# Kernel tuning notes

Measured on AMD Instinct MI355X. Metric: run time of the kernel, lower is better.

The kernel has to match this reference:

```python
import jax, jax.numpy as jnp
import numpy as np

N, D = 512, 256          # n candidates, span_emb_size
R = 4                    # num relation types / etypes
FF = 512                 # mention_linker_ffnn_size, depth 1
L = 2                    # ieg_bignn_hidden_layers
DH = D // 2              # GraphConvolution output size


def setup_inputs() -> dict:
    key = jax.random.key(0)
    ks = jax.random.split(key, 12)
    s = lambda fan_in: 1.0 / np.sqrt(fan_in)
    return {
        "candidate_embs": jax.random.normal(ks[0], (N, D), jnp.float32),
        # relation scorer FFNN: 3D -> FF -> R
        "W_sc0": jax.random.normal(ks[1], (3 * D, FF), jnp.float32) * s(3 * D),
        "b_sc0": jnp.zeros((FF,), jnp.float32),
        "W_sc1": jax.random.normal(ks[2], (FF, R), jnp.float32) * s(FF),
        "b_sc1": jnp.zeros((R,), jnp.float32),
        # BiGCN: per-layer, per-relation fw/bw GraphConvolution D -> D//2
        "W_fw": jax.random.normal(ks[3], (L, R, D, DH), jnp.float32) * s(D),
        "b_fw": jnp.zeros((L, R, DH), jnp.float32),
        "W_bw": jax.random.normal(ks[4], (L, R, D, DH), jnp.float32) * s(D),
        "b_bw": jnp.zeros((L, R, DH), jnp.float32),
        # per-layer linear1: D -> D
        "W_lin": jax.random.normal(ks[5], (L, D, D), jnp.float32) * s(D),
        "b_lin": jnp.zeros((L, D), jnp.float32),
    }


def reference(candidate_embs, W_sc0, b_sc0, W_sc1, b_sc1,
              W_fw, b_fw, W_bw, b_bw, W_lin, b_lin):
    n, d = candidate_embs.shape
    # --- get_pair_embs: [n, n, 3d] = cat(src, target, src*target) ---
    src = jnp.broadcast_to(candidate_embs[None, :, :], (n, n, d))   # row i varies j
    tgt = jnp.broadcast_to(candidate_embs[:, None, :], (n, n, d))
    pair = jnp.concatenate([src, tgt, src * tgt], axis=-1)          # [n, n, 3d]
    # --- relation scorer FFNN (ReLU hidden, dropout=0 at inference) ---
    h = jax.nn.relu(jnp.einsum('ijk,kf->ijf', pair, W_sc0) + b_sc0)
    scores = jnp.einsum('ijf,fr->ijr', h, W_sc1) + b_sc1            # [n, n, R]
    probs = jax.nn.softmax(scores, axis=-1)
    # --- adjs_from_preds: detach, zero diagonal; bw = fw^T ---
    probs = jax.lax.stop_gradient(probs)
    A = jnp.moveaxis(probs, -1, 0)                                   # [R, n, n]
    eye = jnp.eye(n, dtype=bool)
    A = jnp.where(eye[None, :, :], 0.0, A)
    AT = jnp.swapaxes(A, 1, 2)
    # --- BiGCN: L layers of multi-relation bi-directional GCN ---
    x = candidate_embs
    for l in range(L):
        sup_fw = jnp.einsum('nd,rde->rne', x, W_fw[l])               # [R, n, DH]
        sup_bw = jnp.einsum('nd,rde->rne', x, W_bw[l])
        fw = jnp.einsum('rij,rje->rie', A, sup_fw) + b_fw[l][:, None, :]
        bw = jnp.einsum('rij,rje->rie', AT, sup_bw) + b_bw[l][:, None, :]
        outs = jnp.concatenate([bw, fw], axis=-1)                    # [R, n, D]
        x = jax.nn.relu(outs.sum(axis=0)) @ W_lin[l] + b_lin[l] + x  # residual
    return x
```

## Files before the change

kernel.cpp:

```cpp
#include <hip/hip_runtime.h>
#include <hip/hip_bf16.h>

using f32x4  = __attribute__((ext_vector_type(4))) float;
using bf16x8 = __attribute__((ext_vector_type(8))) short;

__device__ __forceinline__ unsigned short f2bf(float f) {
    union { __hip_bfloat16 h; unsigned short u; } cv;
    cv.h = __float2bfloat16(f);
    return cv.u;
}
__device__ __forceinline__ unsigned int pack2bf(float lo, float hi) {
    float2 t; t.x = lo; t.y = hi;
    union { __hip_bfloat162 h; unsigned int u; } cv;
    cv.h = __float22bfloat162_rn(t);
    return cv.u;
}
__device__ __forceinline__ float bf2f(unsigned short u) {
    return __uint_as_float((unsigned)u << 16);
}
__device__ __forceinline__ void ld_lds16(const unsigned short* g, unsigned short* l) {
    __builtin_amdgcn_global_load_lds(
        (const __attribute__((address_space(1))) unsigned int*)g,
        (__attribute__((address_space(3))) unsigned int*)l, 16, 0, 0);
}

__global__ __launch_bounds__(512) void prep_kernel(
        const float* __restrict__ E, const float* __restrict__ Wsc0, const float* __restrict__ Wsc1,
        const float* __restrict__ Wfw, const float* __restrict__ bfw,
        const float* __restrict__ Wbw, const float* __restrict__ bbw,
        const float* __restrict__ Wlin,
        unsigned short* __restrict__ E16, unsigned short* __restrict__ W0p,
        unsigned short* __restrict__ WabP,
        unsigned short* __restrict__ WcatT, unsigned short* __restrict__ WlinT,
        float* __restrict__ bsumS, unsigned short* __restrict__ W1p) {
    const int NE = 131072, NW0 = 131072, NWAB = 262144, NCAT = 524288, NLIN = 131072, NW1P = 8192;
    const int total = NE + NW0 + NWAB + NCAT + NLIN + NW1P + 512;
    for (int idx = blockIdx.x * 512 + threadIdx.x; idx < total; idx += 512 * 512) {
        int t = idx;
        if (t < NE) { E16[t] = f2bf(E[t]); continue; }
        t -= NE;
        if (t < NW0) {
            int k = t >> 9, f = t & 511;
            int w = f >> 6, nb = (f >> 4) & 3, l15 = f & 15;
            int kk = k >> 5, l4 = (k >> 3) & 3, e = k & 7;
            W0p[((((w * 4 + nb) * 8 + kk) * 64) + l4 * 16 + l15) * 8 + e] = f2bf(Wsc0[(512 + k) * 512 + f]);
            continue;
        }
        t -= NW0;
        if (t < NWAB) {
            int r = t >> 9, col = t & 511;
            int k = r & 255;
            int fcol = (r < 256) ? col : (512 + col);
            int wf = fcol >> 6, nb = (fcol >> 4) & 3, l15 = fcol & 15;
            int kk = k >> 5, l4 = (k >> 3) & 3, e = k & 7;
            WabP[((((wf * 4 + nb) * 8 + kk) * 64) + l4 * 16 + l15) * 8 + e] = f2bf(Wsc0[r * 512 + col]);
            continue;
        }
        t -= NWAB;
        if (t < NCAT) {
            int e = t & 127, k = (t >> 7) & 255, r = (t >> 15) & 3, d = (t >> 17) & 1, l = t >> 18;
            const float* src = (d == 0) ? Wfw : Wbw;
            float v = src[((l * 4 + r) * 256 + k) * 128 + e];
            WcatT[(l * 1024 + d * 512 + r * 128 + e) * 256 + k] = f2bf(v);
            continue;
        }
        t -= NCAT;
        if (t < NLIN) {
            int d = t & 255, f = (t >> 8) & 255, l = t >> 16;
            WlinT[(l * 256 + d) * 256 + f] = f2bf(Wlin[(l * 256 + f) * 256 + d]);
            continue;
        }
        t -= NLIN;
        if (t < NW1P) {
            int e = t & 7, lane = (t >> 3) & 63, kap = t >> 9;
            int fp = kap * 32 + (lane >> 4) * 8 + e;
            int w = fp >> 6, q = (fp >> 2) & 15, nb = fp & 3;
            int f = w * 64 + nb * 16 + q;
            int r = lane & 15;
            W1p[t] = (r < 4) ? f2bf(Wsc1[f * 4 + r]) : (unsigned short)0;
            continue;
        }
        t -= NW1P;
        {
            int f = t & 255, l = t >> 8;
            float s = 0.f;
            if (f < 128) { for (int r = 0; r < 4; ++r) s += bbw[(l * 4 + r) * 128 + f]; }
            else         { for (int r = 0; r < 4; ++r) s += bfw[(l * 4 + r) * 128 + (f - 128)]; }
            bsumS[l * 256 + f] = s;
        }
    }
}

__global__ __launch_bounds__(512) void uv_kernel(const unsigned short* __restrict__ E16,
                                                 const unsigned short* __restrict__ WabP,
                                                 const float* __restrict__ bsc0,
                                                 unsigned short* __restrict__ Upk,
                                                 float* __restrict__ V) {
    __shared__ unsigned short sE[32 * 256];
    const int jt = blockIdx.x;
    const int tid = threadIdx.x, lane = tid & 63, w = tid >> 6;
    const int l15 = lane & 15, l4 = lane >> 4;
#pragma unroll
    for (int it = 0; it < 2; ++it) {
        int u = it * 512 + tid;
        int row = u >> 5, slot = u & 31;
        uint4 v = *(const uint4*)(E16 + (jt * 32 + row) * 256 + slot * 8);
        *(uint4*)((char*)sE + row * 512 + ((slot * 16) ^ ((row & 7) << 4))) = v;
    }
    __syncthreads();
    const bf16x8* Wab8 = (const bf16x8*)WabP;
    f32x4 acc[2][8];
#pragma unroll
    for (int a_ = 0; a_ < 2; ++a_)
#pragma unroll
        for (int b_ = 0; b_ < 8; ++b_) acc[a_][b_] = (f32x4){0.f, 0.f, 0.f, 0.f};
#pragma unroll
    for (int kk = 0; kk < 8; ++kk) {
        bf16x8 af[2];
#pragma unroll
        for (int mbl = 0; mbl < 2; ++mbl) {
            int row = mbl * 16 + l15;
            af[mbl] = *(const bf16x8*)((char*)sE + row * 512 + ((kk * 64 + l4 * 16) ^ ((row & 7) << 4)));
        }
#pragma unroll
        for (int nb = 0; nb < 8; ++nb) {
            int wf = 2 * w + (nb >> 2);
            bf16x8 bfr = Wab8[((wf * 4 + (nb & 3)) * 8 + kk) * 64 + lane];
#pragma unroll
            for (int mbl = 0; mbl < 2; ++mbl)
                acc[mbl][nb] = __builtin_amdgcn_mfma_f32_16x16x32_bf16(af[mbl], bfr, acc[mbl][nb], 0, 0, 0);
        }
    }
#pragma unroll
    for (int mbl = 0; mbl < 2; ++mbl) {
        int j_base = jt * 32 + mbl * 16 + l4 * 4;
#pragma unroll
        for (int nb8 = 0; nb8 < 8; ++nb8) {
            int f_g = (2 * w + (nb8 >> 2)) * 64 + (nb8 & 3) * 16 + l15;
            if (f_g < 512) {
                float b0f = bsc0[f_g];
                ushort4 o;
                o.x = f2bf(acc[mbl][nb8][0] + b0f);
                o.y = f2bf(acc[mbl][nb8][1] + b0f);
                o.z = f2bf(acc[mbl][nb8][2] + b0f);
                o.w = f2bf(acc[mbl][nb8][3] + b0f);
                int jtp = j_base >> 6, mbp = (j_base >> 4) & 3;
                int wp = f_g >> 6, nbp = (f_g >> 4) & 3;
                int lanep = l4 * 16 + l15;
                *(ushort4*)(Upk + ((((jtp * 8 + wp) * 4 + mbp) * 2 + (nbp >> 1)) * 64 + lanep) * 8 + (nbp & 1) * 4) = o;
            } else {
                int fv = f_g - 512;
#pragma unroll
                for (int reg = 0; reg < 4; ++reg)
                    V[(j_base + reg) * 512 + fv] = acc[mbl][nb8][reg];
            }
        }
    }
}

__global__ __launch_bounds__(512, 2) void pair_kernel(
    const unsigned short* __restrict__ E16, const unsigned short* __restrict__ W0p,
    const unsigned short* __restrict__ Upk, const float* __restrict__ V,
    const unsigned short* __restrict__ W1p, const float* __restrict__ b1,
    unsigned short* __restrict__ A16) {

    __shared__ unsigned short bufL[2 * 64 * 256];
    __shared__ unsigned short Bbuf[2][8][4][512];
    __shared__ float vrow[2][512];
    __shared__ float scoresL[2][256];

    const int i0 = blockIdx.x * 2, i1 = i0 + 1;
    const int jt = blockIdx.y;
    const int j0 = jt * 64;
    const int tid = threadIdx.x;
    const int lane = tid & 63;
    const int w = tid >> 6;
    const int l15 = lane & 15, l4 = lane >> 4;

    uint4 uq[4][2];
#pragma unroll
    for (int mb = 0; mb < 4; ++mb)
#pragma unroll
        for (int nbh = 0; nbh < 2; ++nbh)
            uq[mb][nbh] = *(const uint4*)(Upk + ((((jt * 8 + w) * 4 + mb) * 2 + nbh) * 64 + lane) * 8);
    vrow[0][tid] = V[i0 * 512 + tid];
    vrow[1][tid] = V[i1 * 512 + tid];
    if (tid < 256) { scoresL[0][tid] = b1[tid & 3]; scoresL[1][tid] = b1[tid & 3]; }

    {
        int m = tid >> 3;
        int s = tid & 7;
        const bf16x8* ejp  = (const bf16x8*)(E16 + (j0 + m) * 256 + s * 8);
        const bf16x8* ei0p = (const bf16x8*)(E16 + i0 * 256 + s * 8);
        const bf16x8* ei1p = (const bf16x8*)(E16 + i1 * 256 + s * 8);
        char* base = (char*)bufL;
#pragma unroll
        for (int c = 0; c < 4; ++c) {
            bf16x8 ej = ejp[c * 8], e0 = ei0p[c * 8], e1 = ei1p[c * 8];
            uint4 v0, v1;
            unsigned* p0 = (unsigned*)&v0;
            unsigned* p1 = (unsigned*)&v1;
#pragma unroll
            for (int e2 = 0; e2 < 4; ++e2) {
                float jl = bf2f((unsigned short)ej[e2 * 2]), jh = bf2f((unsigned short)ej[e2 * 2 + 1]);
                p0[e2] = pack2bf(jl * bf2f((unsigned short)e0[e2 * 2]), jh * bf2f((unsigned short)e0[e2 * 2 + 1]));
                p1[e2] = pack2bf(jl * bf2f((unsigned short)e1[e2 * 2]), jh * bf2f((unsigned short)e1[e2 * 2 + 1]));
            }
            int off = m * 512 + ((s * 16 + c * 128) ^ ((m & 7) << 4));
            *(uint4*)(base + off) = v0;
            *(uint4*)(base + 32768 + off) = v1;
        }
    }

    f32x4 acc0[4][4], acc1[4][4];
#pragma unroll
    for (int mb = 0; mb < 4; ++mb)
#pragma unroll
        for (int nbh = 0; nbh < 2; ++nbh) {
            const unsigned short* us = (const unsigned short*)&uq[mb][nbh];
#pragma unroll
            for (int h = 0; h < 2; ++h) {
                int nb = nbh * 2 + h;
                float v0f = vrow[0][w * 64 + nb * 16 + l15];
                float v1f = vrow[1][w * 64 + nb * 16 + l15];
#pragma unroll
                for (int reg = 0; reg < 4; ++reg) {
                    float uu = bf2f(us[h * 4 + reg]);
                    acc0[mb][nb][reg] = uu + v0f;
                    acc1[mb][nb][reg] = uu + v1f;
                }
            }
        }
    __syncthreads();

#pragma unroll
    for (int nb = 0; nb < 4; ++nb)
        ld_lds16(W0p + ((((w * 4 + nb) * 8 + 0) * 64) + lane) * 8, &Bbuf[0][w][nb][0]);
#pragma unroll
    for (int nb = 0; nb < 4; ++nb)
        ld_lds16(W0p + ((((w * 4 + nb) * 8 + 1) * 64) + lane) * 8, &Bbuf[1][w][nb][0]);

    const char* pbase = (const char*)bufL;
#define PKK(KK, WSTR)                                                                                  \
    {                                                                                                  \
        asm volatile("s_waitcnt " WSTR ::: "memory");                                                  \
        bf16x8 bfr[4];                                                                                 \
        {                                                                                              \
            const char* bsrc = (const char*)(&Bbuf[(KK) & 1][w][0][0]);                                \
            _Pragma("unroll") for (int nb = 0; nb < 4; ++nb)                                           \
                bfr[nb] = *(const bf16x8*)(bsrc + nb * 1024 + lane * 16);                              \
        }                                                                                              \
        bf16x8 afr[4];                                                                                 \
        _Pragma("unroll") for (int mb = 0; mb < 4; ++mb) {                                             \
            int row = mb * 16 + l15;                                                                   \
            afr[mb] = *(const bf16x8*)(pbase + row * 512 + (((KK) * 64 + l4 * 16) ^ ((row & 7) << 4)));\
        }                                                                                              \
        asm volatile("s_waitcnt lgkmcnt(0)" ::: "memory");                                             \
        __builtin_amdgcn_sched_barrier(0);                                                             \
        if ((KK) < 6) {                                                                                \
            _Pragma("unroll") for (int nb = 0; nb < 4; ++nb)                                           \
                ld_lds16(W0p + ((((w * 4 + nb) * 8 + (KK) + 2) * 64) + lane) * 8,                      \
                         &Bbuf[(KK) & 1][w][nb][0]);                                                   \
        }                                                                                              \
        _Pragma("unroll") for (int mb = 0; mb < 4; ++mb)                                               \
            _Pragma("unroll") for (int nb = 0; nb < 4; ++nb)                                           \
                acc0[mb][nb] = __builtin_amdgcn_mfma_f32_16x16x32_bf16(afr[mb], bfr[nb],               \
                                                                       acc0[mb][nb], 0, 0, 0);        \
        _Pragma("unroll") for (int mb = 0; mb < 4; ++mb) {                                             \
            int row = mb * 16 + l15;                                                                   \
            afr[mb] = *(const bf16x8*)(pbase + 32768 + row * 512 +                                     \
                                       (((KK) * 64 + l4 * 16) ^ ((row & 7) << 4)));                    \
        }                                                                                              \
        _Pragma("unroll") for (int mb = 0; mb < 4; ++mb)                                               \
            _Pragma("unroll") for (int nb = 0; nb < 4; ++nb)                                           \
                acc1[mb][nb] = __builtin_amdgcn_mfma_f32_16x16x32_bf16(afr[mb], bfr[nb],               \
                                                                       acc1[mb][nb], 0, 0, 0);        \
    }
    PKK(0, "vmcnt(4)")
    PKK(1, "vmcnt(4)")
    PKK(2, "vmcnt(4)")
    PKK(3, "vmcnt(4)")
    PKK(4, "vmcnt(4)")
    PKK(5, "vmcnt(4)")
    PKK(6, "vmcnt(4)")
    PKK(7, "vmcnt(0)")
#undef PKK
    __syncthreads();

    char* hb = (char*)bufL;
    const bf16x8* W1p8 = (const bf16x8*)W1p;
    bf16x8 w1f[2];
#pragma unroll
    for (int kl = 0; kl < 2; ++kl) w1f[kl] = W1p8[(w * 2 + kl) * 64 + lane];

#pragma unroll
    for (int ii = 0; ii < 2; ++ii) {
#pragma unroll
        for (int mb = 0; mb < 4; ++mb)
#pragma unroll
            for (int reg = 0; reg < 4; ++reg) {
                int rl = mb * 16 + l4 * 4 + reg;
                f32x4* A = (ii == 0) ? &acc0[mb][0] : &acc1[mb][0];
                float h0 = fmaxf(A[0][reg], 0.f);
                float h1 = fmaxf(A[1][reg], 0.f);
                float h2 = fmaxf(A[2][reg], 0.f);
                float h3 = fmaxf(A[3][reg], 0.f);
                uint2 val;
                val.x = pack2bf(h0, h1);
                val.y = pack2bf(h2, h3);
                *(uint2*)(hb + rl * 1024 + ((w * 128 + l15 * 8) ^ ((rl & 7) << 4))) = val;
            }
        __syncthreads();
        f32x4 accS[4];
#pragma unroll
        for (int mb = 0; mb < 4; ++mb) {
            accS[mb] = (f32x4){0.f, 0.f, 0.f, 0.f};
            int rl = mb * 16 + l15;
#pragma unroll
            for (int kl = 0; kl < 2; ++kl) {
                bf16x8 ha = *(const bf16x8*)(hb + rl * 1024 + (((w * 2 + kl) * 64 + l4 * 16) ^ ((rl & 7) << 4)));
                accS[mb] = __builtin_amdgcn_mfma_f32_16x16x32_bf16(ha, w1f[kl], accS[mb], 0, 0, 0);
            }
        }
        if (l15 < 4) {
#pragma unroll
            for (int mb = 0; mb < 4; ++mb)
#pragma unroll
                for (int reg = 0; reg < 4; ++reg)
                    atomicAdd(&scoresL[ii][(mb * 16 + l4 * 4 + reg) * 4 + l15], accS[mb][reg]);
        }
        __syncthreads();
    }

    if (tid < 128) {
        int ii = tid >> 6, m = tid & 63;
        int j = j0 + m, ic = i0 + ii;
        float s0 = scoresL[ii][m * 4 + 0], s1 = scoresL[ii][m * 4 + 1];
        float sA = scoresL[ii][m * 4 + 2], sB = scoresL[ii][m * 4 + 3];
        float mx = fmaxf(fmaxf(s0, s1), fmaxf(sA, sB));
        float e0 = __expf(s0 - mx), e1 = __expf(s1 - mx), e2 = __expf(sA - mx), e3 = __expf(sB - mx);
        float inv = 1.f / (e0 + e1 + e2 + e3);
        float p_[4] = {e0 * inv, e1 * inv, e2 * inv, e3 * inv};
        if (j == ic) { p_[0] = p_[1] = p_[2] = p_[3] = 0.f; }
#pragma unroll
        for (int r = 0; r < 4; ++r)
            A16[(r * 512 + ic) * 512 + j] = f2bf(p_[r]);
    }
}

template<int K>
__device__ __forceinline__ void stageP(unsigned short* lds, const unsigned short* g, int ldg, int tid) {
    constexpr int SLOTS = K / 8;
#pragma unroll
    for (int it = 0; it < (32 * SLOTS) / 256; ++it) {
        int u = it * 256 + tid;
        int row = u / SLOTS, slot = u % SLOTS;
        uint4 v = *(const uint4*)(g + row * ldg + slot * 8);
        *(uint4*)((char*)lds + row * (K * 2) + ((slot * 16) ^ ((row & 7) << 4))) = v;
    }
}
__device__ __forceinline__ void stage64(unsigned short* lds, const unsigned short* g, int ldg, int tid) {
#pragma unroll
    for (int it = 0; it < 8; ++it) {
        int u = it * 256 + tid;
        int row = u >> 5, slot = u & 31;
        uint4 v = *(const uint4*)(g + row * ldg + slot * 8);
        *(uint4*)((char*)lds + row * 512 + ((slot * 16) ^ ((row & 7) << 4))) = v;
    }
}
template<int K>
__device__ __forceinline__ bf16x8 fragP(const unsigned short* lds, int row, int kc, int l4) {
    return *(const bf16x8*)((const char*)lds + row * (K * 2) + ((((kc * 4 + l4) * 16) ^ ((row & 7) << 4))));
}

__global__ __launch_bounds__(256) void c1_kernel(const unsigned short* __restrict__ WcatT,
                                                 const unsigned short* __restrict__ x16,
                                                 unsigned short* __restrict__ supT,
                                                 const unsigned short* __restrict__ A16,
                                                 unsigned short* __restrict__ AT16, int l) {
    __shared__ unsigned short lA[32 * 256], lB[32 * 256];
    int tid = threadIdx.x;
    if (blockIdx.y >= 16) {
        auto t = (unsigned short(*)[65])lA;
        int job = (blockIdx.y - 16) * 32 + blockIdx.x;
        int r = job >> 6, ty = (job >> 3) & 7, tx = job & 7;
        const unsigned short* src = A16 + (r * 512 + ty * 64) * 512 + tx * 64;
        unsigned short* dst = AT16 + (r * 512 + tx * 64) * 512 + ty * 64;
#pragma unroll
        for (int it = 0; it < 2; ++it) {
            int u = it * 256 + tid, row = u >> 3, c8 = (u & 7) * 8;
            uint4 v = *(const uint4*)(src + row * 512 + c8);
            const unsigned short* p = (const unsigned short*)&v;
#pragma unroll
            for (int e = 0; e < 8; ++e) t[c8 + e][row] = p[e];
        }
        __syncthreads();
#pragma unroll
        for (int it = 0; it < 2; ++it) {
            int u = it * 256 + tid, row = u >> 3, c8 = (u & 7) * 8;
            uint4 v; unsigned short* p = (unsigned short*)&v;
#pragma unroll
            for (int e = 0; e < 8; ++e) p[e] = t[row][c8 + e];
            *(uint4*)(dst + row * 512 + c8) = v;
        }
        return;
    }
    int c0 = blockIdx.x * 32, jt0 = blockIdx.y * 32;
    int lane = tid & 63, w = tid >> 6;
    int wr = (w >> 1) * 16, wc = (w & 1) * 16;
    int l15 = lane & 15, l4 = lane >> 4;
    stageP<256>(lA, WcatT + l * 262144 + c0 * 256, 256, tid);
    stageP<256>(lB, x16 + jt0 * 256, 256, tid);
    __syncthreads();
    f32x4 a0 = {0.f,0.f,0.f,0.f}, a1 = {0.f,0.f,0.f,0.f};
#pragma unroll
    for (int kc = 0; kc < 8; kc += 2) {
        a0 = __builtin_amdgcn_mfma_f32_16x16x32_bf16(fragP<256>(lA, wr + l15, kc, l4),
                                                     fragP<256>(lB, wc + l15, kc, l4), a0, 0, 0, 0);
        a1 = __builtin_amdgcn_mfma_f32_16x16x32_bf16(fragP<256>(lA, wr + l15, kc + 1, l4),
                                                     fragP<256>(lB, wc + l15, kc + 1, l4), a1, 0, 0, 0);
    }
    f32x4 acc = a0 + a1;
#pragma unroll
    for (int reg = 0; reg < 4; ++reg) {
        int c = c0 + wr + l4 * 4 + reg;
        int j = jt0 + wc + l15;
        supT[c * 512 + j] = f2bf(acc[reg]);
    }
}

__global__ __launch_bounds__(256) void c2_kernel(const unsigned short* __restrict__ A16,
                                                 const unsigned short* __restrict__ AT16,
                                                 const unsigned short* __restrict__ supT,
                                                 float* __restrict__ Pc2) {
    __shared__ unsigned short lA[64 * 256], lB[64 * 256];
    int i0 = blockIdx.x * 64, f0 = blockIdx.y * 64;
    int s = blockIdx.z, r = s >> 1, kh = s & 1;
    bool bw = (f0 < 128);
    int e0 = bw ? f0 : (f0 - 128);
    const unsigned short* Am = bw ? AT16 : A16;
    int tid = threadIdx.x, lane = tid & 63, w = tid >> 6;
    int wr = (w >> 1) * 32, wc = (w & 1) * 32;
    int l15 = lane & 15, l4 = lane >> 4;
    stage64(lA, Am + (r * 512 + i0) * 512 + kh * 256, 512, tid);
    stage64(lB, supT + ((bw ? 512 : 0) + r * 128 + e0) * 512 + kh * 256, 512, tid);
    __syncthreads();
    f32x4 acc[2][2];
#pragma unroll
    for (int a_ = 0; a_ < 2; ++a_)
#pragma unroll
        for (int b_ = 0; b_ < 2; ++b_) acc[a_][b_] = (f32x4){0.f, 0.f, 0.f, 0.f};
#pragma unroll
    for (int kc = 0; kc < 8; ++kc) {
        bf16x8 af[2], bf_[2];
#pragma unroll
        for (int mb = 0; mb < 2; ++mb) af[mb] = fragP<256>(lA, wr + mb * 16 + l15, kc, l4);
#pragma unroll
        for (int nb = 0; nb < 2; ++nb) bf_[nb] = fragP<256>(lB, wc + nb * 16 + l15, kc, l4);
#pragma unroll
        for (int mb = 0; mb < 2; ++mb)
#pragma unroll
            for (int nb = 0; nb < 2; ++nb)
                acc[mb][nb] = __builtin_amdgcn_mfma_f32_16x16x32_bf16(af[mb], bf_[nb], acc[mb][nb], 0, 0, 0);
    }
    float* dst = Pc2 + s * 131072;
#pragma unroll
    for (int mb = 0; mb < 2; ++mb)
#pragma unroll
        for (int nb = 0; nb < 2; ++nb)
#pragma unroll
            for (int reg = 0; reg < 4; ++reg)
                dst[(i0 + wr + mb * 16 + l4 * 4 + reg) * 256 + f0 + wc + nb * 16 + l15] = acc[mb][nb][reg];
}

__global__ __launch_bounds__(256) void c3_kernel(const float* __restrict__ Pc2,
                                                 const float* __restrict__ bsumS,
                                                 const unsigned short* __restrict__ WlinT,
                                                 const float* __restrict__ blin,
                                                 const float* __restrict__ xold,
                                                 float* __restrict__ xnew,
                                                 unsigned short* __restrict__ x16out, int l) {
    __shared__ unsigned short lA[32 * 256], lB[32 * 256];
    int i0 = blockIdx.x * 32, d0 = blockIdx.y * 32;
    int tid = threadIdx.x, lane = tid & 63, w = tid >> 6;
    int wr = (w >> 1) * 16, wc = (w & 1) * 16;
    int l15 = lane & 15, l4 = lane >> 4;
#pragma unroll
    for (int g = 0; g < 4; ++g) {
        int u = g * 256 + tid;
        int row = u >> 5, k8 = (u & 31) * 8;
        float s[8] = {0,0,0,0,0,0,0,0};
#pragma unroll
        for (int s8 = 0; s8 < 8; ++s8) {
            const float4* p = (const float4*)(Pc2 + s8 * 131072 + (i0 + row) * 256 + k8);
            float4 a = p[0], b = p[1];
            s[0] += a.x; s[1] += a.y; s[2] += a.z; s[3] += a.w;
            s[4] += b.x; s[5] += b.y; s[6] += b.z; s[7] += b.w;
        }
        uint4 v;
        unsigned* vp = (unsigned*)&v;
#pragma unroll
        for (int e2 = 0; e2 < 4; ++e2) {
            float lo = fmaxf(s[e2 * 2] + bsumS[l * 256 + k8 + e2 * 2], 0.f);
            float hi = fmaxf(s[e2 * 2 + 1] + bsumS[l * 256 + k8 + e2 * 2 + 1], 0.f);
            vp[e2] = pack2bf(lo, hi);
        }
        *(uint4*)((char*)lA + row * 512 + ((k8 * 2) ^ ((row & 7) << 4))) = v;
    }
    stageP<256>(lB, WlinT + l * 65536 + d0 * 256, 256, tid);
    __syncthreads();
    f32x4 a0 = {0.f,0.f,0.f,0.f}, a1 = {0.f,0.f,0.f,0.f};
#pragma unroll
    for (int kc = 0; kc < 8; kc += 2) {
        a0 = __builtin_amdgcn_mfma_f32_16x16x32_bf16(fragP<256>(lA, wr + l15, kc, l4),
                                                     fragP<256>(lB, wc + l15, kc, l4), a0, 0, 0, 0);
        a1 = __builtin_amdgcn_mfma_f32_16x16x32_bf16(fragP<256>(lA, wr + l15, kc + 1, l4),
                                                     fragP<256>(lB, wc + l15, kc + 1, l4), a1, 0, 0, 0);
    }
    f32x4 acc = a0 + a1;
#pragma unroll
    for (int reg = 0; reg < 4; ++reg) {
        int ii = i0 + wr + l4 * 4 + reg;
        int dd = d0 + wc + l15;
        float vv = acc[reg] + blin[l * 256 + dd] + xold[ii * 256 + dd];
        xnew[ii * 256 + dd] = vv;
        x16out[ii * 256 + dd] = f2bf(vv);
    }
}

extern "C" void kernel_launch(void* const* d_in, const int* in_sizes, int n_in,
                              void* d_out, int out_size, void* d_ws, size_t ws_size,
                              hipStream_t stream) {
    const float* E    = (const float*)d_in[0];
    const float* Wsc0 = (const float*)d_in[1];
    const float* bsc0 = (const float*)d_in[2];
    const float* Wsc1 = (const float*)d_in[3];
    const float* bsc1 = (const float*)d_in[4];
    const float* Wfw  = (const float*)d_in[5];
    const float* bfw  = (const float*)d_in[6];
    const float* Wbw  = (const float*)d_in[7];
    const float* bbw  = (const float*)d_in[8];
    const float* Wlin = (const float*)d_in[9];
    const float* blin = (const float*)d_in[10];
    float* out = (float*)d_out;

    char* ws = (char*)d_ws;
    size_t off = 0;
    unsigned short* E16   = (unsigned short*)(ws + off); off += 512 * 256 * 2;
    unsigned short* W0p   = (unsigned short*)(ws + off); off += 512 * 256 * 2;
    unsigned short* WabP  = (unsigned short*)(ws + off); off += 1024 * 256 * 2;
    unsigned short* WcatT = (unsigned short*)(ws + off); off += 2 * 1024 * 256 * 2;
    unsigned short* WlinT = (unsigned short*)(ws + off); off += 2 * 256 * 256 * 2;
    float* bsumS          = (float*)(ws + off);          off += 2 * 256 * 4;
    unsigned short* Upk   = (unsigned short*)(ws + off); off += 512 * 512 * 2;
    float* V              = (float*)(ws + off);          off += 512 * 512 * 4;
    unsigned short* W1p   = (unsigned short*)(ws + off); off += 16 * 64 * 8 * 2;
    unsigned short* A16   = (unsigned short*)(ws + off); off += 4 * 512 * 512 * 2;
    unsigned short* AT16  = (unsigned short*)(ws + off); off += 4 * 512 * 512 * 2;
    unsigned short* supT  = (unsigned short*)(ws + off); off += 1024 * 512 * 2;
    float* Pc2            = (float*)(ws + off);          off += 8 * 512 * 256 * 4;
    float* xf1            = (float*)(ws + off);          off += 512 * 256 * 4;
    unsigned short* x16_1 = (unsigned short*)(ws + off); off += 512 * 256 * 2;

    prep_kernel<<<512, 512, 0, stream>>>(E, Wsc0, Wsc1, Wfw, bfw, Wbw, bbw, Wlin,
                                         E16, W0p, WabP, WcatT, WlinT, bsumS, W1p);
    uv_kernel<<<16, 512, 0, stream>>>(E16, WabP, bsc0, Upk, V);
    pair_kernel<<<dim3(256, 8), 512, 0, stream>>>(E16, W0p, Upk, V, W1p, bsc1, A16);

    for (int l = 0; l < 2; ++l) {
        const unsigned short* xin16 = (l == 0) ? E16 : x16_1;
        const float* xoldf = (l == 0) ? E : xf1;
        float* xout = (l == 0) ? xf1 : out;
        c1_kernel<<<dim3(32, (l == 0) ? 24 : 16), 256, 0, stream>>>(WcatT, xin16, supT, A16, AT16, l);
        c2_kernel<<<dim3(8, 4, 8), 256, 0, stream>>>(A16, AT16, supT, Pc2);
        c3_kernel<<<dim3(16, 8), 256, 0, stream>>>(Pc2, bsumS, WlinT, blin, xoldf, xout, x16_1, l);
    }
    (void)in_sizes; (void)n_in; (void)out_size; (void)ws_size;
}
```

Measured before the change: 192.8 us.

## Double pair_kernel block to 1024 threads with shared W0 tile staging

After: 228.2 us. 1.18x slower.

```diff
diff --git a/kernel.cpp b/kernel.cpp
--- a/kernel.cpp
+++ b/kernel.cpp
@@ -158,14 +158,14 @@
     }
 }
 
-__global__ __launch_bounds__(512, 2) void pair_kernel(
+__global__ __launch_bounds__(1024) void pair_kernel(
     const unsigned short* __restrict__ E16, const unsigned short* __restrict__ W0p,
     const unsigned short* __restrict__ Upk, const float* __restrict__ V,
     const unsigned short* __restrict__ W1p, const float* __restrict__ b1,
     unsigned short* __restrict__ A16) {
 
     __shared__ unsigned short bufL[2 * 64 * 256];
-    __shared__ unsigned short Bbuf[2][8][4][512];
+    __shared__ unsigned short Bsh[2][32 * 512];
     __shared__ float vrow[2][512];
     __shared__ float scoresL[2][256];
 
@@ -174,55 +174,58 @@
     const int j0 = jt * 64;
     const int tid = threadIdx.x;
     const int lane = tid & 63;
-    const int w = tid >> 6;
+    const int w16 = tid >> 6;
+    const int fg = w16 & 7;
+    const int jh = w16 >> 3;
     const int l15 = lane & 15, l4 = lane >> 4;
 
-    uint4 uq[4][2];
-#pragma unroll
-    for (int mb = 0; mb < 4; ++mb)
+    uint4 uq[2][2];
+#pragma unroll
+    for (int mb = 0; mb < 2; ++mb)
 #pragma unroll
         for (int nbh = 0; nbh < 2; ++nbh)
-            uq[mb][nbh] = *(const uint4*)(Upk + ((((jt * 8 + w) * 4 + mb) * 2 + nbh) * 64 + lane) * 8);
-    vrow[0][tid] = V[i0 * 512 + tid];
-    vrow[1][tid] = V[i1 * 512 + tid];
+            uq[mb][nbh] = *(const uint4*)(Upk +
+                ((((jt * 8 + fg) * 4 + (jh * 2 + mb)) * 2 + nbh) * 64 + lane) * 8);
+    if (tid < 512) vrow[0][tid] = V[i0 * 512 + tid];
+    else           vrow[1][tid - 512] = V[i1 * 512 + (tid - 512)];
     if (tid < 256) { scoresL[0][tid] = b1[tid & 3]; scoresL[1][tid] = b1[tid & 3]; }
 
     {
-        int m = tid >> 3;
-        int s = tid & 7;
+        int m = tid >> 4;
+        int s = tid & 15;
         const bf16x8* ejp  = (const bf16x8*)(E16 + (j0 + m) * 256 + s * 8);
         const bf16x8* ei0p = (const bf16x8*)(E16 + i0 * 256 + s * 8);
         const bf16x8* ei1p = (const bf16x8*)(E16 + i1 * 256 + s * 8);
         char* base = (char*)bufL;
 #pragma unroll
-        for (int c = 0; c < 4; ++c) {
-            bf16x8 ej = ejp[c * 8], e0 = ei0p[c * 8], e1 = ei1p[c * 8];
+        for (int c = 0; c < 2; ++c) {
+            bf16x8 ej = ejp[c * 16], e0 = ei0p[c * 16], e1 = ei1p[c * 16];
             uint4 v0, v1;
             unsigned* p0 = (unsigned*)&v0;
             unsigned* p1 = (unsigned*)&v1;
 #pragma unroll
             for (int e2 = 0; e2 < 4; ++e2) {
-                float jl = bf2f((unsigned short)ej[e2 * 2]), jh = bf2f((unsigned short)ej[e2 * 2 + 1]);
-                p0[e2] = pack2bf(jl * bf2f((unsigned short)e0[e2 * 2]), jh * bf2f((unsigned short)e0[e2 * 2 + 1]));
-                p1[e2] = pack2bf(jl * bf2f((unsigned short)e1[e2 * 2]), jh * bf2f((unsigned short)e1[e2 * 2 + 1]));
+                float jl = bf2f((unsigned short)ej[e2 * 2]), jh_ = bf2f((unsigned short)ej[e2 * 2 + 1]);
+                p0[e2] = pack2bf(jl * bf2f((unsigned short)e0[e2 * 2]), jh_ * bf2f((unsigned short)e0[e2 * 2 + 1]));
+                p1[e2] = pack2bf(jl * bf2f((unsigned short)e1[e2 * 2]), jh_ * bf2f((unsigned short)e1[e2 * 2 + 1]));
             }
-            int off = m * 512 + ((s * 16 + c * 128) ^ ((m & 7) << 4));
+            int off = m * 512 + (((s + c * 16) * 16) ^ ((m & 7) << 4));
             *(uint4*)(base + off) = v0;
             *(uint4*)(base + 32768 + off) = v1;
         }
     }
 
-    f32x4 acc0[4][4], acc1[4][4];
-#pragma unroll
-    for (int mb = 0; mb < 4; ++mb)
+    f32x4 acc0[2][4], acc1[2][4];
+#pragma unroll
+    for (int mb = 0; mb < 2; ++mb)
 #pragma unroll
         for (int nbh = 0; nbh < 2; ++nbh) {
             const unsigned short* us = (const unsigned short*)&uq[mb][nbh];
 #pragma unroll
             for (int h = 0; h < 2; ++h) {
                 int nb = nbh * 2 + h;
-                float v0f = vrow[0][w * 64 + nb * 16 + l15];
-                float v1f = vrow[1][w * 64 + nb * 16 + l15];
+                float v0f = vrow[0][fg * 64 + nb * 16 + l15];
+                float v1f = vrow[1][fg * 64 + nb * 16 + l15];
 #pragma unroll
                 for (int reg = 0; reg < 4; ++reg) {
                     float uu = bf2f(us[h * 4 + reg]);
@@ -231,75 +234,70 @@
                 }
             }
         }
+
+#pragma unroll
+    for (int cc = 0; cc < 2; ++cc) {
+        int c = 2 * w16 + cc;
+        ld_lds16(W0p + ((c * 8 + 0) * 64 + lane) * 8, &Bsh[0][c * 512]);
+    }
     __syncthreads();
-
-#pragma unroll
-    for (int nb = 0; nb < 4; ++nb)
-        ld_lds16(W0p + ((((w * 4 + nb) * 8 + 0) * 64) + lane) * 8, &Bbuf[0][w][nb][0]);
-#pragma unroll
-    for (int nb = 0; nb < 4; ++nb)
-        ld_lds16(W0p + ((((w * 4 + nb) * 8 + 1) * 64) + lane) * 8, &Bbuf[1][w][nb][0]);
 
     const char* pbase = (const char*)bufL;
 #define PKK(KK, WSTR)                                                                                  \
     {                                                                                                  \
+        if ((KK) < 7) {                                                                                \
+            _Pragma("unroll") for (int cc = 0; cc < 2; ++cc) {                                         \
+                int c = 2 * w16 + cc;                                                                  \
+                ld_lds16(W0p + ((c * 8 + (KK) + 1) * 64 + lane) * 8, &Bsh[((KK) + 1) & 1][c * 512]);   \
+            }                                                                                          \
+        }                                                                                              \
         asm volatile("s_waitcnt " WSTR ::: "memory");                                                  \
+        asm volatile("s_barrier" ::: "memory");                                                        \
         bf16x8 bfr[4];                                                                                 \
-        {                                                                                              \
-            const char* bsrc = (const char*)(&Bbuf[(KK) & 1][w][0][0]);                                \
-            _Pragma("unroll") for (int nb = 0; nb < 4; ++nb)                                           \
-                bfr[nb] = *(const bf16x8*)(bsrc + nb * 1024 + lane * 16);                              \
-        }                                                                                              \
-        bf16x8 afr[4];                                                                                 \
-        _Pragma("unroll") for (int mb = 0; mb < 4; ++mb) {                                             \
-            int row = mb * 16 + l15;                                                                   \
+        _Pragma("unroll") for (int nb = 0; nb < 4; ++nb)                                               \
+            bfr[nb] = *(const bf16x8*)(&Bsh[(KK) & 1][(fg * 4 + nb) * 512] + lane * 8);                \
+        bf16x8 afr[2];                                                                                 \
+        _Pragma("unroll") for (int mb = 0; mb < 2; ++mb) {                                             \
+            int row = jh * 32 + mb * 16 + l15;                                                         \
             afr[mb] = *(const bf16x8*)(pbase + row * 512 + (((KK) * 64 + l4 * 16) ^ ((row & 7) << 4)));\
         }                                                                                              \
-        asm volatile("s_waitcnt lgkmcnt(0)" ::: "memory");                                             \
-        __builtin_amdgcn_sched_barrier(0);                                                             \
-        if ((KK) < 6) {                                                                                \
-            _Pragma("unroll") for (int nb = 0; nb < 4; ++nb)                                           \
-                ld_lds16(W0p + ((((w * 4 + nb) * 8 + (KK) + 2) * 64) + lane) * 8,                      \
-                         &Bbuf[(KK) & 1][w][nb][0]);                                                   \
-        }                                                                                              \
-        _Pragma("unroll") for (int mb = 0; mb < 4; ++mb)                                               \
+        _Pragma("unroll") for (int mb = 0; mb < 2; ++mb)                                               \
             _Pragma("unroll") for (int nb = 0; nb < 4; ++nb)                                           \
                 acc0[mb][nb] = __builtin_amdgcn_mfma_f32_16x16x32_bf16(afr[mb], bfr[nb],               \
                                                                        acc0[mb][nb], 0, 0, 0);        \
-        _Pragma("unroll") for (int mb = 0; mb < 4; ++mb) {                                             \
-            int row = mb * 16 + l15;                                                                   \
+        _Pragma("unroll") for (int mb = 0; mb < 2; ++mb) {                                             \
+            int row = jh * 32 + mb * 16 + l15;                                                         \
             afr[mb] = *(const bf16x8*)(pbase + 32768 + row * 512 +                                     \
                                        (((KK) * 64 + l4 * 16) ^ ((row & 7) << 4)));                    \
         }                                                                                              \
-        _Pragma("unroll") for (int mb = 0; mb < 4; ++mb)                                               \
+        _Pragma("unroll") for (int mb = 0; mb < 2; ++mb)                                               \
             _Pragma("unroll") for (int nb = 0; nb < 4; ++nb)                                           \
                 acc1[mb][nb] = __builtin_amdgcn_mfma_f32_16x16x32_bf16(afr[mb], bfr[nb],               \
                                                                        acc1[mb][nb], 0, 0, 0);        \
-    }
-    PKK(0, "vmcnt(4)")
-    PKK(1, "vmcnt(4)")
-    PKK(2, "vmcnt(4)")
-    PKK(3, "vmcnt(4)")
-    PKK(4, "vmcnt(4)")
-    PKK(5, "vmcnt(4)")
-    PKK(6, "vmcnt(4)")
+        asm volatile("s_barrier" ::: "memory");                                                        \
+    }
+    PKK(0, "vmcnt(2)")
+    PKK(1, "vmcnt(2)")
+    PKK(2, "vmcnt(2)")
+    PKK(3, "vmcnt(2)")
+    PKK(4, "vmcnt(2)")
+    PKK(5, "vmcnt(2)")
+    PKK(6, "vmcnt(2)")
     PKK(7, "vmcnt(0)")
 #undef PKK
     __syncthreads();
 
     char* hb = (char*)bufL;
     const bf16x8* W1p8 = (const bf16x8*)W1p;
-    bf16x8 w1f[2];
-#pragma unroll
-    for (int kl = 0; kl < 2; ++kl) w1f[kl] = W1p8[(w * 2 + kl) * 64 + lane];
+    bf16x8 w1f = W1p8[w16 * 64 + lane];
 
 #pragma unroll
     for (int ii = 0; ii < 2; ++ii) {
 #pragma unroll
-        for (int mb = 0; mb < 4; ++mb)
+        for (int mb = 0; mb < 2; ++mb)
 #pragma unroll
             for (int reg = 0; reg < 4; ++reg) {
-                int rl = mb * 16 + l4 * 4 + reg;
+                int rl = jh * 32 + mb * 16 + l4 * 4 + reg;
                 f32x4* A = (ii == 0) ? &acc0[mb][0] : &acc1[mb][0];
                 float h0 = fmaxf(A[0][reg], 0.f);
                 float h1 = fmaxf(A[1][reg], 0.f);
@@ -308,26 +306,23 @@
                 uint2 val;
                 val.x = pack2bf(h0, h1);
                 val.y = pack2bf(h2, h3);
-                *(uint2*)(hb + rl * 1024 + ((w * 128 + l15 * 8) ^ ((rl & 7) << 4))) = val;
+                *(uint2*)(hb + rl * 1024 + ((fg * 128 + l15 * 8) ^ ((rl & 7) << 4))) = val;
             }
         __syncthreads();
         f32x4 accS[4];
 #pragma unroll
-        for (int mb = 0; mb < 4; ++mb) {
-            accS[mb] = (f32x4){0.f, 0.f, 0.f, 0.f};
-            int rl = mb * 16 + l15;
-#pragma unroll
-            for (int kl = 0; kl < 2; ++kl) {
-                bf16x8 ha = *(const bf16x8*)(hb + rl * 1024 + (((w * 2 + kl) * 64 + l4 * 16) ^ ((rl & 7) << 4)));
-                accS[mb] = __builtin_amdgcn_mfma_f32_16x16x32_bf16(ha, w1f[kl], accS[mb], 0, 0, 0);
-            }
+        for (int mbS = 0; mbS < 4; ++mbS) {
+            accS[mbS] = (f32x4){0.f, 0.f, 0.f, 0.f};
+            int rl = mbS * 16 + l15;
+            bf16x8 ha = *(const bf16x8*)(hb + rl * 1024 + ((w16 * 64 + l4 * 16) ^ ((rl & 7) << 4)));
+            accS[mbS] = __builtin_amdgcn_mfma_f32_16x16x32_bf16(ha, w1f, accS[mbS], 0, 0, 0);
         }
         if (l15 < 4) {
 #pragma unroll
-            for (int mb = 0; mb < 4; ++mb)
+            for (int mbS = 0; mbS < 4; ++mbS)
 #pragma unroll
                 for (int reg = 0; reg < 4; ++reg)
-                    atomicAdd(&scoresL[ii][(mb * 16 + l4 * 4 + reg) * 4 + l15], accS[mb][reg]);
+                    atomicAdd(&scoresL[ii][(mbS * 16 + l4 * 4 + reg) * 4 + l15], accS[mbS][reg]);
         }
         __syncthreads();
     }
@@ -565,7 +560,7 @@
     prep_kernel<<<512, 512, 0, stream>>>(E, Wsc0, Wsc1, Wfw, bfw, Wbw, bbw, Wlin,
                                          E16, W0p, WabP, WcatT, WlinT, bsumS, W1p);
     uv_kernel<<<16, 512, 0, stream>>>(E16, WabP, bsc0, Upk, V);
-    pair_kernel<<<dim3(256, 8), 512, 0, stream>>>(E16, W0p, Upk, V, W1p, bsc1, A16);
+    pair_kernel<<<dim3(256, 8), 1024, 0, stream>>>(E16, W0p, Upk, V, W1p, bsc1, A16);
 
     for (int l = 0; l < 2; ++l) {
         const unsigned short* xin16 = (l == 0) ? E16 : x16_1;
```
